# Kernel optimization log

Hardware: AMD Instinct MI355X
Metric: run time of the kernel (lower is better)

## Reference

```python
import jax, jax.numpy as jnp
import numpy as np

D_MODEL = 512
N_HEADS = 8
D_K = D_MODEL // N_HEADS
WINDOW = 64
SCALE = 1.0 / np.sqrt(D_K)


def setup_inputs() -> dict:
    key = jax.random.key(0)
    ks = jax.random.split(key, 9)
    B, S = 1, 2048
    s = 1.0 / np.sqrt(D_MODEL)
    inp = {
        "x": jax.random.normal(ks[0], (B, S, D_MODEL), dtype=jnp.float32),
        "Wq": jax.random.normal(ks[1], (D_MODEL, D_MODEL), dtype=jnp.float32) * s,
        "bq": jnp.zeros((D_MODEL,), dtype=jnp.float32),
        "Wk": jax.random.normal(ks[2], (D_MODEL, D_MODEL), dtype=jnp.float32) * s,
        "bk": jnp.zeros((D_MODEL,), dtype=jnp.float32),
        "Wv": jax.random.normal(ks[3], (D_MODEL, D_MODEL), dtype=jnp.float32) * s,
        "bv": jnp.zeros((D_MODEL,), dtype=jnp.float32),
        "Wo": jax.random.normal(ks[4], (D_MODEL, D_MODEL), dtype=jnp.float32) * s,
        "bo": jnp.zeros((D_MODEL,), dtype=jnp.float32),
    }
    return inp


def reference(x, Wq, bq, Wk, bk, Wv, bv, Wo, bo):
    B, S, _ = x.shape
    # projections (torch Linear: x @ W.T + b); split heads -> [B,S,H,dk]
    q = (x @ Wq.T + bq).reshape(B, S, N_HEADS, D_K)
    k = (x @ Wk.T + bk).reshape(B, S, N_HEADS, D_K)
    v = (x @ Wv.T + bv).reshape(B, S, N_HEADS, D_K)

    # banded window indices: position i attends to [i-W, i+W]
    L = 2 * WINDOW + 1
    offsets = jnp.arange(L) - WINDOW                    # [L]
    pos = jnp.arange(S)[:, None] + offsets[None, :]     # [S, L]
    valid = (pos >= 0) & (pos < S)                      # [S, L]
    posc = jnp.clip(pos, 0, S - 1)

    k_w = k[:, posc]                                    # [B, S, L, H, dk]
    v_w = v[:, posc]                                    # [B, S, L, H, dk]

    scores = jnp.einsum("bshd,bslhd->bhsl", q, k_w) * SCALE
    scores = jnp.where(valid[None, None, :, :], scores, -jnp.inf)
    attn = jax.nn.softmax(scores, axis=-1)              # [B, H, S, L]
    out = jnp.einsum("bhsl,bslhd->bshd", attn, v_w)     # [B, S, H, dk]
    out = out.reshape(B, S, D_MODEL)
    return out @ Wo.T + bo
```

## Files before the change

### kernel.cpp

```cpp
#include <hip/hip_runtime.h>
#include <hip/hip_bf16.h>
#include <math.h>

#define S_LEN  2048
#define DMODEL 512
#define NHEADS 8
#define DK     64
#define WIN    64

static constexpr float SCALE = 0.125f;

typedef short bf16x8 __attribute__((ext_vector_type(8)));
typedef float f32x4  __attribute__((ext_vector_type(4)));

__device__ __forceinline__ short bfh(float v)
{
    __hip_bfloat16 b = __float2bfloat16(v);
    return *reinterpret_cast<short*>(&b);
}
__device__ __forceinline__ float bf2f(short s)
{
    __hip_bfloat16 b = *reinterpret_cast<__hip_bfloat16*>(&s);
    return __bfloat162float(b);
}
__device__ __forceinline__ void split1(float v, short& h, short& l)
{
    h = bfh(v);
    l = bfh(v - bf2f(h));
}

__device__ __forceinline__ void dma16(const void* g, void* l)
{
    __builtin_amdgcn_global_load_lds(
        (const __attribute__((address_space(1))) unsigned int*)g,
        (__attribute__((address_space(3))) unsigned int*)l, 16, 0, 0);
}

__global__ __launch_bounds__(256)
void cast_ws(const float* __restrict__ x,  const float* __restrict__ wq,
             const float* __restrict__ wk, const float* __restrict__ wv,
             const float* __restrict__ wo,
             short* __restrict__ xh, short* __restrict__ xl,
             short* __restrict__ wqb, short* __restrict__ wkb,
             short* __restrict__ wvb, short* __restrict__ wob)
{
    const int z = blockIdx.z;
    if (z == 0) {
        for (int i = blockIdx.x * 256 + threadIdx.x; i < 262144; i += gridDim.x * 256) {
            const float4 v = ((const float4*)x)[i];
            short4 h, l;
            split1(v.x, h.x, l.x);
            split1(v.y, h.y, l.y);
            split1(v.z, h.z, l.z);
            split1(v.w, h.w, l.w);
            ((short4*)xh)[i] = h;
            ((short4*)xl)[i] = l;
        }
    } else {
        const float* s; short* d;
        switch (z) {
            case 1:  s = wq; d = wqb; break;
            case 2:  s = wk; d = wkb; break;
            case 3:  s = wv; d = wvb; break;
            default: s = wo; d = wob; break;
        }
        for (int i = blockIdx.x * 256 + threadIdx.x; i < 65536; i += gridDim.x * 256) {
            const float4 v = ((const float4*)s)[i];
            short4 o;
            o.x = bfh(v.x); o.y = bfh(v.y); o.z = bfh(v.z); o.w = bfh(v.w);
            ((short4*)d)[i] = o;
        }
    }
}

template<int BM, int BN, int MT, int NT>
__device__ __forceinline__ void gemm2_acc(const short* __restrict__ Ahg,
                                          const short* __restrict__ Alg,
                                          const short* __restrict__ Bg,
                                          int row0, int col0,
                                          f32x4 acc[MT][NT])
{
    __shared__ __align__(16) short sAh[BM * 32];
    __shared__ __align__(16) short sAl[BM * 32];
    __shared__ __align__(16) short sB [BN * 32];

    const int tid  = threadIdx.x;
    const int lane = tid & 63;
    const int wv   = tid >> 6;
    const int col  = lane & 15;
    const int quad = lane >> 4;
    const int wm0  = (wv >> 1) * (MT * 16);
    const int wn0  = (wv & 1) * (NT * 16);
    const int lr   = lane >> 2;
    const int lc   = lane & 3;
    constexpr int nIss = (2 * BM + BN) / 16;

#pragma unroll
    for (int i = 0; i < MT; ++i)
#pragma unroll
        for (int j = 0; j < NT; ++j)
            acc[i][j] = (f32x4)0.0f;

    for (int k0 = 0; k0 < 512; k0 += 32) {
        __syncthreads();
        for (int i = wv; i < nIss; i += 4) {
            const short* src; short* dst; int grp, ro;
            if (i < BM / 16)          { grp = i;            src = Ahg; dst = sAh; ro = row0; }
            else if (i < BM / 8)      { grp = i - BM / 16;  src = Alg; dst = sAl; ro = row0; }
            else                      { grp = i - BM / 8;   src = Bg;  dst = sB;  ro = col0; }
            const int r  = grp * 16 + lr;
            const int cs = lc ^ ((r >> 1) & 3);
            dma16(src + (size_t)(ro + r) * 512 + k0 + cs * 8, dst + grp * 512);
        }
        __syncthreads();

        bf16x8 fh[MT], fl[MT], fb[NT];
#pragma unroll
        for (int mi = 0; mi < MT; ++mi) {
            const int m = wm0 + mi * 16 + col;
            const int p = quad ^ ((m >> 1) & 3);
            fh[mi] = *(const bf16x8*)&sAh[m * 32 + p * 8];
            fl[mi] = *(const bf16x8*)&sAl[m * 32 + p * 8];
        }
#pragma unroll
        for (int nj = 0; nj < NT; ++nj) {
            const int n = wn0 + nj * 16 + col;
            const int p = quad ^ ((n >> 1) & 3);
            fb[nj] = *(const bf16x8*)&sB[n * 32 + p * 8];
        }
#pragma unroll
        for (int mi = 0; mi < MT; ++mi)
#pragma unroll
            for (int nj = 0; nj < NT; ++nj) {
                acc[mi][nj] = __builtin_amdgcn_mfma_f32_16x16x32_bf16(fh[mi], fb[nj], acc[mi][nj], 0, 0, 0);
                acc[mi][nj] = __builtin_amdgcn_mfma_f32_16x16x32_bf16(fl[mi], fb[nj], acc[mi][nj], 0, 0, 0);
            }
    }
}

__global__ __launch_bounds__(256)
void gemm_qkv2(const short* __restrict__ xh, const short* __restrict__ xl,
               const short* __restrict__ wqb, const short* __restrict__ wkb,
               const short* __restrict__ wvb,
               const float* __restrict__ bq, const float* __restrict__ bk,
               const float* __restrict__ bv,
               short* __restrict__ qh, short* __restrict__ ql,
               short* __restrict__ kb, short* __restrict__ vb)
{
    const int z = blockIdx.z;
    const short* B; const float* bias;
    if (z == 0)      { B = wqb; bias = bq; }
    else if (z == 1) { B = wkb; bias = bk; }
    else             { B = wvb; bias = bv; }
    const int row0 = blockIdx.y * 64, col0 = blockIdx.x * 64;

    f32x4 acc[2][2];
    gemm2_acc<64, 64, 2, 2>(xh, xl, B, row0, col0, acc);

    const int tid  = threadIdx.x;
    const int lane = tid & 63;
    const int wv   = tid >> 6;
    const int col  = lane & 15;
    const int quad = lane >> 4;
    const int wm0  = (wv >> 1) * 32;
    const int wn0  = (wv & 1) * 32;

#pragma unroll
    for (int nj = 0; nj < 2; ++nj) {
        const int cc = col0 + wn0 + nj * 16 + col;
        const float bias_v = bias[cc];
#pragma unroll
        for (int mi = 0; mi < 2; ++mi) {
#pragma unroll
            for (int e = 0; e < 4; ++e) {
                const int row = row0 + wm0 + mi * 16 + quad * 4 + e;
                const float val = acc[mi][nj][e] + bias_v;
                const size_t idx = (size_t)row * 512 + cc;
                if (z == 0) {
                    short hh, ll;
                    split1(val, hh, ll);
                    qh[idx] = hh;
                    ql[idx] = ll;
                } else if (z == 1) {
                    kb[idx] = bfh(val);
                } else {
                    vb[idx] = bfh(val);
                }
            }
        }
    }
}

__global__ __launch_bounds__(256)
void gemm_out2(const short* __restrict__ ah, const short* __restrict__ al,
               const short* __restrict__ wob, const float* __restrict__ bo,
               float* __restrict__ out)
{
    const int row0 = blockIdx.y * 32, col0 = blockIdx.x * 64;
    f32x4 acc[1][2];
    gemm2_acc<32, 64, 1, 2>(ah, al, wob, row0, col0, acc);

    const int tid  = threadIdx.x;
    const int lane = tid & 63;
    const int wv   = tid >> 6;
    const int col  = lane & 15;
    const int quad = lane >> 4;
    const int wm0  = (wv >> 1) * 16;
    const int wn0  = (wv & 1) * 32;

#pragma unroll
    for (int nj = 0; nj < 2; ++nj) {
        const int cc = col0 + wn0 + nj * 16 + col;
        const float bias_v = bo[cc];
#pragma unroll
        for (int e = 0; e < 4; ++e) {
            const int row = row0 + wm0 + quad * 4 + e;
            out[(size_t)row * 512 + cc] = acc[0][nj][e] + bias_v;
        }
    }
}

__global__ __launch_bounds__(256)
void banded_attn2(const short* __restrict__ qh, const short* __restrict__ ql,
                  const short* __restrict__ kb, const short* __restrict__ vb,
                  short* __restrict__ abh, short* __restrict__ abl)
{
    __shared__ __align__(16) short VtS[64 * 200];
    __shared__ __align__(16) short KS [192 * 64];
    __shared__ __align__(16) short QhS[32 * 64];
    __shared__ __align__(16) short QlS[32 * 64];
    __shared__ float pmax[4][32];
    __shared__ float psum[4][32];
    short* PS = KS;

    const int h    = blockIdx.x;
    const int t0   = blockIdx.y * 32;
    const int tid  = threadIdx.x;
    const int lane = tid & 63;
    const int wv   = tid >> 6;
    const int col  = lane & 15;
    const int quad = lane >> 4;

    {
        const int lr = lane >> 3;
        const int lc = lane & 7;
        for (int i = wv; i < 32; i += 4) {
            const short* src; short* dst; int r;
            if (i < 4) {
                r = i * 8 + lr;
                src = qh + (size_t)(t0 + r) * 512 + h * 64;
                dst = QhS + i * 512;
            } else if (i < 8) {
                const int g = i - 4;
                r = g * 8 + lr;
                src = ql + (size_t)(t0 + r) * 512 + h * 64;
                dst = QlS + g * 512;
            } else {
                const int g = i - 8;
                r = g * 8 + lr;
                int pos = t0 - 64 + r;
                pos = pos < 0 ? 0 : (pos > 2047 ? 2047 : pos);
                src = kb + (size_t)pos * 512 + h * 64;
                dst = KS + g * 512;
            }
            const int cs = lc ^ (r & 7);
            dma16(src + cs * 8, dst);
        }
    }
#pragma unroll
    for (int ch = 0; ch < 3; ++ch) {
        const int pr  = ch * 64 + lane;
        int pos = t0 - 64 + pr;
        pos = pos < 0 ? 0 : (pos > 2047 ? 2047 : pos);
#pragma unroll
        for (int c = 0; c < 4; ++c) {
            const int d0 = wv * 16 + c * 4;
            const short4 v = *(const short4*)(vb + (size_t)pos * 512 + h * 64 + d0);
            VtS[(d0 + 0) * 200 + pr] = v.x;
            VtS[(d0 + 1) * 200 + pr] = v.y;
            VtS[(d0 + 2) * 200 + pr] = v.z;
            VtS[(d0 + 3) * 200 + pr] = v.w;
        }
    }
    __syncthreads();

    f32x4 sacc[2][3];
#pragma unroll
    for (int mi = 0; mi < 2; ++mi)
#pragma unroll
        for (int nj = 0; nj < 3; ++nj)
            sacc[mi][nj] = (f32x4)0.0f;

#pragma unroll
    for (int ks = 0; ks < 2; ++ks) {
        const int q0 = ks * 4 + quad;
        bf16x8 aqh[2], aql[2];
#pragma unroll
        for (int mi = 0; mi < 2; ++mi) {
            const int m = mi * 16 + col;
            const int p = q0 ^ (m & 7);
            aqh[mi] = *(const bf16x8*)&QhS[m * 64 + p * 8];
            aql[mi] = *(const bf16x8*)&QlS[m * 64 + p * 8];
        }
#pragma unroll
        for (int nj = 0; nj < 3; ++nj) {
            const int n = wv * 48 + nj * 16 + col;
            const int p = q0 ^ (n & 7);
            const bf16x8 bkf = *(const bf16x8*)&KS[n * 64 + p * 8];
#pragma unroll
            for (int mi = 0; mi < 2; ++mi) {
                sacc[mi][nj] = __builtin_amdgcn_mfma_f32_16x16x32_bf16(aqh[mi], bkf, sacc[mi][nj], 0, 0, 0);
                sacc[mi][nj] = __builtin_amdgcn_mfma_f32_16x16x32_bf16(aql[mi], bkf, sacc[mi][nj], 0, 0, 0);
            }
        }
    }

    float pv[2][3][4];
#pragma unroll
    for (int mi = 0; mi < 2; ++mi)
#pragma unroll
        for (int nj = 0; nj < 3; ++nj)
#pragma unroll
            for (int e = 0; e < 4; ++e) {
                const int r32 = mi * 16 + quad * 4 + e;
                const int n   = wv * 48 + nj * 16 + col;
                const int pos = t0 - 64 + n;
                const int d   = n - r32;
                const bool valid = (pos >= 0) && (pos < S_LEN) && (d >= 0) && (d <= 128);
                pv[mi][nj][e] = valid ? sacc[mi][nj][e] * SCALE : -__builtin_inff();
            }

#pragma unroll
    for (int mi = 0; mi < 2; ++mi)
#pragma unroll
        for (int e = 0; e < 4; ++e) {
            float mx = fmaxf(fmaxf(pv[mi][0][e], pv[mi][1][e]), pv[mi][2][e]);
#pragma unroll
            for (int off = 1; off < 16; off <<= 1)
                mx = fmaxf(mx, __shfl_xor(mx, off));
            if ((lane & 15) == 0) pmax[wv][mi * 16 + quad * 4 + e] = mx;
        }
    __syncthreads();

#pragma unroll
    for (int mi = 0; mi < 2; ++mi)
#pragma unroll
        for (int e = 0; e < 4; ++e) {
            const int r32 = mi * 16 + quad * 4 + e;
            const float m = fmaxf(fmaxf(pmax[0][r32], pmax[1][r32]),
                                  fmaxf(pmax[2][r32], pmax[3][r32]));
            float ss = 0.f;
#pragma unroll
            for (int nj = 0; nj < 3; ++nj) {
                const float p = __expf(pv[mi][nj][e] - m);
                pv[mi][nj][e] = p;
                ss += p;
            }
#pragma unroll
            for (int off = 1; off < 16; off <<= 1)
                ss += __shfl_xor(ss, off);
            if ((lane & 15) == 0) psum[wv][r32] = ss;
#pragma unroll
            for (int nj = 0; nj < 3; ++nj) {
                const int n = wv * 48 + nj * 16 + col;
                PS[r32 * 200 + n] = bfh(pv[mi][nj][e]);
            }
        }
    __syncthreads();

    const int mi = wv >> 1;
    f32x4 oacc[2];
    oacc[0] = (f32x4)0.0f;
    oacc[1] = (f32x4)0.0f;
#pragma unroll
    for (int ks = 0; ks < 6; ++ks) {
        const bf16x8 pa = *(const bf16x8*)&PS[(mi * 16 + col) * 200 + ks * 32 + quad * 8];
#pragma unroll
        for (int t = 0; t < 2; ++t) {
            const int nj = (wv & 1) * 2 + t;
            const bf16x8 vf = *(const bf16x8*)&VtS[(nj * 16 + col) * 200 + ks * 32 + quad * 8];
            oacc[t] = __builtin_amdgcn_mfma_f32_16x16x32_bf16(pa, vf, oacc[t], 0, 0, 0);
        }
    }

    float linv[4];
#pragma unroll
    for (int e = 0; e < 4; ++e) {
        const int r32 = mi * 16 + quad * 4 + e;
        linv[e] = 1.0f / (psum[0][r32] + psum[1][r32] + psum[2][r32] + psum[3][r32]);
    }
#pragma unroll
    for (int t = 0; t < 2; ++t) {
        const int nj = (wv & 1) * 2 + t;
#pragma unroll
        for (int e = 0; e < 4; ++e) {
            const int r32 = mi * 16 + quad * 4 + e;
            const float val = oacc[t][e] * linv[e];
            short hh, ll;
            split1(val, hh, ll);
            const size_t idx = (size_t)(t0 + r32) * 512 + h * 64 + nj * 16 + col;
            abh[idx] = hh;
            abl[idx] = ll;
        }
    }
}

extern "C" void kernel_launch(void* const* d_in, const int* in_sizes, int n_in,
                              void* d_out, int out_size, void* d_ws, size_t ws_size,
                              hipStream_t stream)
{
    const float* x  = (const float*)d_in[0];
    const float* Wq = (const float*)d_in[1];
    const float* bq = (const float*)d_in[2];
    const float* Wk = (const float*)d_in[3];
    const float* bk = (const float*)d_in[4];
    const float* Wv = (const float*)d_in[5];
    const float* bv = (const float*)d_in[6];
    const float* Wo = (const float*)d_in[7];
    const float* bo = (const float*)d_in[8];
    float* out = (float*)d_out;

    char* ws = (char*)d_ws;
    short* qh  = (short*)(ws);
    short* ql  = (short*)(ws + (2u << 20));
    short* kb  = (short*)(ws + (4u << 20));
    short* vb  = (short*)(ws + (6u << 20));
    short* xh  = (short*)(ws + (8u << 20));
    short* xl  = (short*)(ws + (10u << 20));
    short* wqb = (short*)(ws + (12u << 20));
    short* wkb = (short*)(ws + (12u << 20) + 1 * (512u << 10));
    short* wvb = (short*)(ws + (12u << 20) + 2 * (512u << 10));
    short* wob = (short*)(ws + (12u << 20) + 3 * (512u << 10));
    short* abh = xh;
    short* abl = xl;

    dim3 gc(128, 1, 5);
    cast_ws<<<gc, 256, 0, stream>>>(x, Wq, Wk, Wv, Wo,
                                    xh, xl, wqb, wkb, wvb, wob);

    dim3 gq(DMODEL / 64, S_LEN / 64, 3);
    gemm_qkv2<<<gq, 256, 0, stream>>>(xh, xl, wqb, wkb, wvb,
                                      bq, bk, bv, qh, ql, kb, vb);

    dim3 ga(NHEADS, S_LEN / 32);
    banded_attn2<<<ga, 256, 0, stream>>>(qh, ql, kb, vb, abh, abl);

    dim3 go(DMODEL / 64, S_LEN / 32);
    gemm_out2<<<go, 256, 0, stream>>>(abh, abl, wob, bo, out);
}
```

Measured before the change: 118.6 us.

## Restructure projection GEMMs and store V transposed for DMA-based attention loads

The QKV and output GEMMs are rewritten as 128-thread blocks. Each block stages a 64x256 half of the weight tile in LDS with XOR swizzling (two phases instead of sixteen k-steps) and reads the activation hi/lo fragments straight from global memory, which cuts the number of barriers. The V projection now writes a transposed [d][seq] layout. This lets the attention kernel load its V tile with 16-byte async DMA into a swizzled LDS buffer instead of scalar transposing stores. The costs are uncoalesced scattered stores when writing transposed V, and A-fragment loads that bypass LDS and may be re-read across blocks.

```diff
diff --git a/kernel.cpp b/kernel.cpp
--- a/kernel.cpp
+++ b/kernel.cpp
@@ -73,159 +73,161 @@
     }
 }
 
-template<int BM, int BN, int MT, int NT>
-__device__ __forceinline__ void gemm2_acc(const short* __restrict__ Ahg,
-                                          const short* __restrict__ Alg,
-                                          const short* __restrict__ Bg,
-                                          int row0, int col0,
-                                          f32x4 acc[MT][NT])
-{
-    __shared__ __align__(16) short sAh[BM * 32];
-    __shared__ __align__(16) short sAl[BM * 32];
-    __shared__ __align__(16) short sB [BN * 32];
-
+__global__ __launch_bounds__(128)
+void gemm_qkv3(const short* __restrict__ xh, const short* __restrict__ xl,
+               const short* __restrict__ wqb, const short* __restrict__ wkb,
+               const short* __restrict__ wvb,
+               const float* __restrict__ bq, const float* __restrict__ bk,
+               const float* __restrict__ bv,
+               short* __restrict__ qh, short* __restrict__ ql,
+               short* __restrict__ kb, short* __restrict__ vbt)
+{
+    __shared__ __align__(16) short sB[64 * 256];
+
+    const int z = blockIdx.z;
+    const short* Bg   = (z == 0) ? wqb : (z == 1) ? wkb : wvb;
+    const float* bias = (z == 0) ? bq  : (z == 1) ? bk  : bv;
+    const int row0 = blockIdx.y * 64;
+    const int col0 = blockIdx.x * 64;
     const int tid  = threadIdx.x;
     const int lane = tid & 63;
     const int wv   = tid >> 6;
     const int col  = lane & 15;
     const int quad = lane >> 4;
-    const int wm0  = (wv >> 1) * (MT * 16);
-    const int wn0  = (wv & 1) * (NT * 16);
-    const int lr   = lane >> 2;
-    const int lc   = lane & 3;
-    constexpr int nIss = (2 * BM + BN) / 16;
-
-#pragma unroll
-    for (int i = 0; i < MT; ++i)
-#pragma unroll
-        for (int j = 0; j < NT; ++j)
-            acc[i][j] = (f32x4)0.0f;
-
-    for (int k0 = 0; k0 < 512; k0 += 32) {
+
+    f32x4 acc[2][4];
+#pragma unroll
+    for (int mi = 0; mi < 2; ++mi)
+#pragma unroll
+        for (int nj = 0; nj < 4; ++nj)
+            acc[mi][nj] = (f32x4)0.0f;
+
+    for (int ph = 0; ph < 2; ++ph) {
         __syncthreads();
-        for (int i = wv; i < nIss; i += 4) {
-            const short* src; short* dst; int grp, ro;
-            if (i < BM / 16)          { grp = i;            src = Ahg; dst = sAh; ro = row0; }
-            else if (i < BM / 8)      { grp = i - BM / 16;  src = Alg; dst = sAl; ro = row0; }
-            else                      { grp = i - BM / 8;   src = Bg;  dst = sB;  ro = col0; }
-            const int r  = grp * 16 + lr;
-            const int cs = lc ^ ((r >> 1) & 3);
-            dma16(src + (size_t)(ro + r) * 512 + k0 + cs * 8, dst + grp * 512);
+        for (int i = wv; i < 32; i += 2) {
+            const int q = i * 64 + lane;
+            const int r = q >> 5;
+            const int b = q & 31;
+            const int j = b ^ (r & 7);
+            dma16(Bg + (size_t)(col0 + r) * 512 + ph * 256 + j * 8, sB + i * 512);
         }
         __syncthreads();
 
-        bf16x8 fh[MT], fl[MT], fb[NT];
-#pragma unroll
-        for (int mi = 0; mi < MT; ++mi) {
-            const int m = wm0 + mi * 16 + col;
-            const int p = quad ^ ((m >> 1) & 3);
-            fh[mi] = *(const bf16x8*)&sAh[m * 32 + p * 8];
-            fl[mi] = *(const bf16x8*)&sAl[m * 32 + p * 8];
-        }
-#pragma unroll
-        for (int nj = 0; nj < NT; ++nj) {
-            const int n = wn0 + nj * 16 + col;
-            const int p = quad ^ ((n >> 1) & 3);
-            fb[nj] = *(const bf16x8*)&sB[n * 32 + p * 8];
-        }
-#pragma unroll
-        for (int mi = 0; mi < MT; ++mi)
-#pragma unroll
-            for (int nj = 0; nj < NT; ++nj) {
-                acc[mi][nj] = __builtin_amdgcn_mfma_f32_16x16x32_bf16(fh[mi], fb[nj], acc[mi][nj], 0, 0, 0);
-                acc[mi][nj] = __builtin_amdgcn_mfma_f32_16x16x32_bf16(fl[mi], fb[nj], acc[mi][nj], 0, 0, 0);
-            }
-    }
-}
-
-__global__ __launch_bounds__(256)
-void gemm_qkv2(const short* __restrict__ xh, const short* __restrict__ xl,
-               const short* __restrict__ wqb, const short* __restrict__ wkb,
-               const short* __restrict__ wvb,
-               const float* __restrict__ bq, const float* __restrict__ bk,
-               const float* __restrict__ bv,
-               short* __restrict__ qh, short* __restrict__ ql,
-               short* __restrict__ kb, short* __restrict__ vb)
-{
-    const int z = blockIdx.z;
-    const short* B; const float* bias;
-    if (z == 0)      { B = wqb; bias = bq; }
-    else if (z == 1) { B = wkb; bias = bk; }
-    else             { B = wvb; bias = bv; }
-    const int row0 = blockIdx.y * 64, col0 = blockIdx.x * 64;
-
-    f32x4 acc[2][2];
-    gemm2_acc<64, 64, 2, 2>(xh, xl, B, row0, col0, acc);
-
+#pragma unroll
+        for (int kc = 0; kc < 8; ++kc) {
+            const int k = ph * 256 + kc * 32;
+            bf16x8 ah[2], al[2];
+#pragma unroll
+            for (int mi = 0; mi < 2; ++mi) {
+                const int m = row0 + wv * 32 + mi * 16 + col;
+                ah[mi] = *(const bf16x8*)(xh + (size_t)m * 512 + k + quad * 8);
+                al[mi] = *(const bf16x8*)(xl + (size_t)m * 512 + k + quad * 8);
+            }
+#pragma unroll
+            for (int nj = 0; nj < 4; ++nj) {
+                const int n = nj * 16 + col;
+                const int j = (kc * 4 + quad) ^ (n & 7);
+                const bf16x8 bf = *(const bf16x8*)&sB[n * 256 + j * 8];
+#pragma unroll
+                for (int mi = 0; mi < 2; ++mi) {
+                    acc[mi][nj] = __builtin_amdgcn_mfma_f32_16x16x32_bf16(ah[mi], bf, acc[mi][nj], 0, 0, 0);
+                    acc[mi][nj] = __builtin_amdgcn_mfma_f32_16x16x32_bf16(al[mi], bf, acc[mi][nj], 0, 0, 0);
+                }
+            }
+        }
+    }
+
+#pragma unroll
+    for (int nj = 0; nj < 4; ++nj) {
+        const int cc = col0 + nj * 16 + col;
+        const float bias_v = bias[cc];
+#pragma unroll
+        for (int mi = 0; mi < 2; ++mi) {
+#pragma unroll
+            for (int e = 0; e < 4; ++e) {
+                const int row = row0 + wv * 32 + mi * 16 + quad * 4 + e;
+                const float val = acc[mi][nj][e] + bias_v;
+                if (z == 0) {
+                    short hh, ll;
+                    split1(val, hh, ll);
+                    qh[(size_t)row * 512 + cc] = hh;
+                    ql[(size_t)row * 512 + cc] = ll;
+                } else if (z == 1) {
+                    kb[(size_t)row * 512 + cc] = bfh(val);
+                } else {
+                    vbt[(size_t)cc * 2048 + row] = bfh(val);
+                }
+            }
+        }
+    }
+}
+
+__global__ __launch_bounds__(128)
+void gemm_out3(const short* __restrict__ ah_g, const short* __restrict__ al_g,
+               const short* __restrict__ wob, const float* __restrict__ bo,
+               float* __restrict__ out)
+{
+    __shared__ __align__(16) short sB[64 * 256];
+
+    const int row0 = blockIdx.y * 32;
+    const int col0 = blockIdx.x * 64;
     const int tid  = threadIdx.x;
     const int lane = tid & 63;
     const int wv   = tid >> 6;
     const int col  = lane & 15;
     const int quad = lane >> 4;
-    const int wm0  = (wv >> 1) * 32;
-    const int wn0  = (wv & 1) * 32;
-
-#pragma unroll
-    for (int nj = 0; nj < 2; ++nj) {
-        const int cc = col0 + wn0 + nj * 16 + col;
-        const float bias_v = bias[cc];
-#pragma unroll
-        for (int mi = 0; mi < 2; ++mi) {
-#pragma unroll
-            for (int e = 0; e < 4; ++e) {
-                const int row = row0 + wm0 + mi * 16 + quad * 4 + e;
-                const float val = acc[mi][nj][e] + bias_v;
-                const size_t idx = (size_t)row * 512 + cc;
-                if (z == 0) {
-                    short hh, ll;
-                    split1(val, hh, ll);
-                    qh[idx] = hh;
-                    ql[idx] = ll;
-                } else if (z == 1) {
-                    kb[idx] = bfh(val);
-                } else {
-                    vb[idx] = bfh(val);
-                }
-            }
+
+    f32x4 acc[4];
+#pragma unroll
+    for (int nj = 0; nj < 4; ++nj)
+        acc[nj] = (f32x4)0.0f;
+
+    for (int ph = 0; ph < 2; ++ph) {
+        __syncthreads();
+        for (int i = wv; i < 32; i += 2) {
+            const int q = i * 64 + lane;
+            const int r = q >> 5;
+            const int b = q & 31;
+            const int j = b ^ (r & 7);
+            dma16(wob + (size_t)(col0 + r) * 512 + ph * 256 + j * 8, sB + i * 512);
+        }
+        __syncthreads();
+
+#pragma unroll
+        for (int kc = 0; kc < 8; ++kc) {
+            const int k = ph * 256 + kc * 32;
+            const int m = row0 + wv * 16 + col;
+            const bf16x8 ah = *(const bf16x8*)(ah_g + (size_t)m * 512 + k + quad * 8);
+            const bf16x8 al = *(const bf16x8*)(al_g + (size_t)m * 512 + k + quad * 8);
+#pragma unroll
+            for (int nj = 0; nj < 4; ++nj) {
+                const int n = nj * 16 + col;
+                const int j = (kc * 4 + quad) ^ (n & 7);
+                const bf16x8 bf = *(const bf16x8*)&sB[n * 256 + j * 8];
+                acc[nj] = __builtin_amdgcn_mfma_f32_16x16x32_bf16(ah, bf, acc[nj], 0, 0, 0);
+                acc[nj] = __builtin_amdgcn_mfma_f32_16x16x32_bf16(al, bf, acc[nj], 0, 0, 0);
+            }
+        }
+    }
+
+#pragma unroll
+    for (int nj = 0; nj < 4; ++nj) {
+        const int cc = col0 + nj * 16 + col;
+        const float bias_v = bo[cc];
+#pragma unroll
+        for (int e = 0; e < 4; ++e) {
+            const int row = row0 + wv * 16 + quad * 4 + e;
+            out[(size_t)row * 512 + cc] = acc[nj][e] + bias_v;
         }
     }
 }
 
 __global__ __launch_bounds__(256)
-void gemm_out2(const short* __restrict__ ah, const short* __restrict__ al,
-               const short* __restrict__ wob, const float* __restrict__ bo,
-               float* __restrict__ out)
-{
-    const int row0 = blockIdx.y * 32, col0 = blockIdx.x * 64;
-    f32x4 acc[1][2];
-    gemm2_acc<32, 64, 1, 2>(ah, al, wob, row0, col0, acc);
-
-    const int tid  = threadIdx.x;
-    const int lane = tid & 63;
-    const int wv   = tid >> 6;
-    const int col  = lane & 15;
-    const int quad = lane >> 4;
-    const int wm0  = (wv >> 1) * 16;
-    const int wn0  = (wv & 1) * 32;
-
-#pragma unroll
-    for (int nj = 0; nj < 2; ++nj) {
-        const int cc = col0 + wn0 + nj * 16 + col;
-        const float bias_v = bo[cc];
-#pragma unroll
-        for (int e = 0; e < 4; ++e) {
-            const int row = row0 + wm0 + quad * 4 + e;
-            out[(size_t)row * 512 + cc] = acc[0][nj][e] + bias_v;
-        }
-    }
-}
-
-__global__ __launch_bounds__(256)
-void banded_attn2(const short* __restrict__ qh, const short* __restrict__ ql,
-                  const short* __restrict__ kb, const short* __restrict__ vb,
+void banded_attn3(const short* __restrict__ qh, const short* __restrict__ ql,
+                  const short* __restrict__ kb, const short* __restrict__ vbt,
                   short* __restrict__ abh, short* __restrict__ abl)
 {
-    __shared__ __align__(16) short VtS[64 * 200];
+    __shared__ __align__(16) short VtS[64 * 256];
     __shared__ __align__(16) short KS [192 * 64];
     __shared__ __align__(16) short QhS[32 * 64];
     __shared__ __align__(16) short QlS[32 * 64];
@@ -266,20 +268,15 @@
             const int cs = lc ^ (r & 7);
             dma16(src + cs * 8, dst);
         }
-    }
-#pragma unroll
-    for (int ch = 0; ch < 3; ++ch) {
-        const int pr  = ch * 64 + lane;
-        int pos = t0 - 64 + pr;
-        pos = pos < 0 ? 0 : (pos > 2047 ? 2047 : pos);
-#pragma unroll
-        for (int c = 0; c < 4; ++c) {
-            const int d0 = wv * 16 + c * 4;
-            const short4 v = *(const short4*)(vb + (size_t)pos * 512 + h * 64 + d0);
-            VtS[(d0 + 0) * 200 + pr] = v.x;
-            VtS[(d0 + 1) * 200 + pr] = v.y;
-            VtS[(d0 + 2) * 200 + pr] = v.z;
-            VtS[(d0 + 3) * 200 + pr] = v.w;
+        for (int i = wv; i < 32; i += 4) {
+            const int q = i * 64 + lane;
+            const int d = q >> 5;
+            const int b = q & 31;
+            const int j0 = (b < 24) ? b : 0;
+            const int j = j0 ^ (d & 7);
+            int p0 = t0 - 64 + j * 8;
+            p0 = p0 < 0 ? 0 : (p0 > 2040 ? 2040 : p0);
+            dma16(vbt + (size_t)(h * 64 + d) * 2048 + p0, VtS + i * 512);
         }
     }
     __syncthreads();
@@ -377,8 +374,9 @@
         const bf16x8 pa = *(const bf16x8*)&PS[(mi * 16 + col) * 200 + ks * 32 + quad * 8];
 #pragma unroll
         for (int t = 0; t < 2; ++t) {
-            const int nj = (wv & 1) * 2 + t;
-            const bf16x8 vf = *(const bf16x8*)&VtS[(nj * 16 + col) * 200 + ks * 32 + quad * 8];
+            const int d = ((wv & 1) * 2 + t) * 16 + col;
+            const int j = (ks * 4 + quad) ^ (d & 7);
+            const bf16x8 vf = *(const bf16x8*)&VtS[d * 256 + j * 8];
             oacc[t] = __builtin_amdgcn_mfma_f32_16x16x32_bf16(pa, vf, oacc[t], 0, 0, 0);
         }
     }
@@ -424,7 +422,7 @@
     short* qh  = (short*)(ws);
     short* ql  = (short*)(ws + (2u << 20));
     short* kb  = (short*)(ws + (4u << 20));
-    short* vb  = (short*)(ws + (6u << 20));
+    short* vbt = (short*)(ws + (6u << 20));
     short* xh  = (short*)(ws + (8u << 20));
     short* xl  = (short*)(ws + (10u << 20));
     short* wqb = (short*)(ws + (12u << 20));
@@ -439,12 +437,12 @@
                                     xh, xl, wqb, wkb, wvb, wob);
 
     dim3 gq(DMODEL / 64, S_LEN / 64, 3);
-    gemm_qkv2<<<gq, 256, 0, stream>>>(xh, xl, wqb, wkb, wvb,
-                                      bq, bk, bv, qh, ql, kb, vb);
+    gemm_qkv3<<<gq, 128, 0, stream>>>(xh, xl, wqb, wkb, wvb,
+                                      bq, bk, bv, qh, ql, kb, vbt);
 
     dim3 ga(NHEADS, S_LEN / 32);
-    banded_attn2<<<ga, 256, 0, stream>>>(qh, ql, kb, vb, abh, abl);
+    banded_attn3<<<ga, 256, 0, stream>>>(qh, ql, kb, vbt, abh, abl);
 
     dim3 go(DMODEL / 64, S_LEN / 32);
-    gemm_out2<<<go, 256, 0, stream>>>(abh, abl, wob, bo, out);
-}
+    gemm_out3<<<go, 128, 0, stream>>>(abh, abl, wob, bo, out);
+}
```

New measurement: 114.8 us. 3.2% less time.
